# Performance work log

Hardware: AMD Instinct MI355X
Metric: run time of the kernel (lower is better)

The kernel has to match this reference:

```python
import jax, jax.numpy as jnp
import numpy as np

N, K, H, X_DIM, S_DIM = 50000, 8, 128, 32, 27
LSTM_IN = X_DIM + 3 * H  # 416


def setup_inputs() -> dict:
    key = jax.random.key(0)
    ks = jax.random.split(key, 16)

    def u(k, shape, fan_in):
        lim = 1.0 / np.sqrt(fan_in)
        return jax.random.uniform(k, shape, jnp.float32, -lim, lim)

    return {
        "x": jax.random.normal(ks[0], (N, X_DIM), jnp.float32),
        "h_self": jax.random.normal(ks[1], (N, H), jnp.float32),
        "c_self": jax.random.normal(ks[2], (N, H), jnp.float32),
        "h_inflows": jax.random.normal(ks[3], (N, K, H), jnp.float32),
        "inflow_valid": jax.random.randint(ks[4], (N, K), 0, 2) > 0,
        "static": jax.random.normal(ks[5], (N, S_DIM), jnp.float32),
        # Linear weights stored (out, in) as in eqx.nn.Linear
        "Wn": u(ks[6], (H, H), H),                     # W_neighbor, no bias
        "Wg": u(ks[7], (H, 2 * H), 2 * H),             # W_inflow_gate
        "bg": u(ks[8], (H,), 2 * H),
        "Ws": u(ks[9], (H, S_DIM), S_DIM),             # W_static
        "bs": u(ks[10], (H,), S_DIM),
        "Wl": u(ks[11], (4 * H, LSTM_IN), LSTM_IN),    # W_lstm
        "bl": u(ks[12], (4 * H,), LSTM_IN),
        "ln_w": jnp.ones((H,), jnp.float32),           # ln_h affine
        "ln_b": jnp.zeros((H,), jnp.float32),
    }


def reference(x, h_self, c_self, h_inflows, inflow_valid, static,
              Wn, Wg, bg, Ws, bs, Wl, bl, ln_w, ln_b):
    eps = 1e-5
    # per-neighbor message: [N,K,H]
    msgs = jnp.einsum('nkh,oh->nko', h_inflows, Wn)
    # inflow gate on concat(h_inflow, h_self): [N,K,H]
    h_tiled = jnp.broadcast_to(h_self[:, None, :], h_inflows.shape)
    gate_in = jnp.concatenate([h_inflows, h_tiled], axis=-1)  # [N,K,2H]
    gates = jax.nn.sigmoid(jnp.einsum('nkd,od->nko', gate_in, Wg) + bg)
    # masked sum over neighbors -> [N,H]
    mask = inflow_valid[..., None].astype(jnp.float32)
    neighbor_context = jnp.sum(gates * msgs * mask, axis=1)
    static_proj = static @ Ws.T + bs  # [N,H]
    combined = jnp.concatenate([x, h_self, neighbor_context, static_proj], axis=-1)
    z = combined @ Wl.T + bl  # [N,4H]
    i, f, o, g = jnp.split(z, 4, axis=-1)
    c_new = jax.nn.sigmoid(f) * c_self + jax.nn.sigmoid(i) * jnp.tanh(g)
    h_new = jax.nn.sigmoid(o) * jnp.tanh(c_new)
    # LayerNorm over hidden dim (eqx default eps=1e-5, affine)
    mu = jnp.mean(h_new, axis=-1, keepdims=True)
    var = jnp.mean(jnp.square(h_new - mu), axis=-1, keepdims=True)
    h_new = (h_new - mu) * jax.lax.rsqrt(var + eps) * ln_w + ln_b
    return (h_new, c_new)
```

## Files before the change

kernel.cpp:

```cpp
#include <hip/hip_runtime.h>
#include <hip/hip_bf16.h>

#define NN 50000
#define KI 8
#define H 128
#define XD 32
#define SD 27
#define CIN 416
#define CIN2 320
#define CPAD 328
#define ZOUT 512
#define NTILE_NB (NN / KI)
#define MB_LSTM 64

typedef __attribute__((ext_vector_type(8))) short bf16x8;
typedef __attribute__((ext_vector_type(4))) float f32x4;
typedef __attribute__((ext_vector_type(4))) unsigned short us4;

#define MFMA16(a, b, c) __builtin_amdgcn_mfma_f32_16x16x32_bf16((a), (b), (c), 0, 0, 0)

static __device__ __forceinline__ float sigmoidf_(float x) {
    return 1.0f / (1.0f + __expf(-x));
}
static __device__ __forceinline__ unsigned short f2b(float f) {
    union { float f; unsigned int u; } v; v.f = f;
    unsigned int r = v.u + 0x7FFF + ((v.u >> 16) & 1);
    return (unsigned short)(r >> 16);
}
static __device__ __forceinline__ float dot4_(float4 a, float4 b) {
    return a.x * b.x + a.y * b.y + a.z * b.z + a.w * b.w;
}

__global__ __launch_bounds__(256) void k_prep(
    const float* __restrict__ Wn, const float* __restrict__ Wg,
    const float* __restrict__ Wl, const float* __restrict__ bl,
    const float* __restrict__ Ws, const float* __restrict__ bs,
    unsigned short* __restrict__ WnB, unsigned short* __restrict__ WgB,
    unsigned short* __restrict__ WpB, float* __restrict__ bp)
{
    const int b = blockIdx.x, t = threadIdx.x;
    if (b < 512) {
        const float* wr = Wl + (size_t)b * CIN;
        unsigned short* out = WpB + (size_t)b * CIN2;
        for (int c = t; c < CIN2; c += 256) {
            float v;
            if (c < 288) v = wr[c];
            else if (c < 288 + SD) {
                int s = c - 288;
                float acc = 0.f;
                for (int j = 0; j < H; ++j) acc += wr[288 + j] * Ws[j * SD + s];
                v = acc;
            } else v = 0.f;
            out[c] = f2b(v);
        }
        if (t == 0) {
            float acc = bl[b];
            for (int j = 0; j < H; ++j) acc += wr[288 + j] * bs[j];
            bp[b] = acc;
        }
    } else {
        int idx = (b - 512) * 256 + t;
        for (int r = idx; r < 49152; r += 16384) {
            if (r < 16384) WnB[r] = f2b(Wn[r]);
            else WgB[r - 16384] = f2b(Wg[r - 16384]);
        }
    }
}

__global__ __launch_bounds__(256, 2) void k_nb_mfma(
    const float* __restrict__ hself_g, const float* __restrict__ hin_g,
    const unsigned char* __restrict__ valid_raw,
    const unsigned short* __restrict__ WnB, const unsigned short* __restrict__ WgB,
    const float* __restrict__ bg,
    unsigned short* __restrict__ ncb, int nc_stride)
{
    __shared__ unsigned short hin_s[64 * 128];
    __shared__ unsigned short hs_s[8 * 128];
    __shared__ float gh_s[8][128];
    __shared__ unsigned short ncs[8 * 128];
    __shared__ float valid_s[64];

    const int t = threadIdx.x;
    const int w = t >> 6, l = t & 63;
    const int ln = l & 15, lk = l >> 4;

    int det = 0;
    #pragma unroll
    for (int i = 0; i < 64; ++i) det |= valid_raw[4 * i + 1];
    const bool f8 = (det != 0);

    bf16x8 Bn[2][4], Ba[2][4], Bb[2][4];
    const int cbase = w * 32;
    #pragma unroll
    for (int c = 0; c < 2; ++c) {
        const int col = cbase + c * 16 + ln;
        #pragma unroll
        for (int kk = 0; kk < 4; ++kk) {
            const int k0 = kk * 32 + lk * 8;
            Bn[c][kk] = *(const bf16x8*)(WnB + col * H + k0);
            Ba[c][kk] = *(const bf16x8*)(WgB + col * 2 * H + k0);
            Bb[c][kk] = *(const bf16x8*)(WgB + col * 2 * H + H + k0);
        }
    }
    const float bg0 = bg[cbase + ln];
    const float bg1 = bg[cbase + 16 + ln];

    for (int tile = blockIdx.x; tile < NTILE_NB; tile += gridDim.x) {
        const int nb = tile * 8;

        if (t < 64) {
            bool v = f8 ? (valid_raw[(size_t)nb * KI + t] != 0)
                        : (((const unsigned int*)valid_raw)[(size_t)nb * KI + t] != 0u);
            valid_s[t] = v ? 1.f : 0.f;
        }
        {
            const float4* src = (const float4*)(hin_g + (size_t)nb * KI * H);
            float4 r0[8];
            #pragma unroll
            for (int i = 0; i < 8; ++i) r0[i] = src[t + i * 256];
            float4 hv = ((const float4*)(hself_g + (size_t)nb * H))[t];
            #pragma unroll
            for (int i = 0; i < 8; ++i) {
                int e = (t + i * 256) * 4, row = e >> 7, col = e & 127;
                unsigned byte = (unsigned)(row * 256 + col * 2) ^ (unsigned)((row & 7) << 4);
                us4 pk = { f2b(r0[i].x), f2b(r0[i].y), f2b(r0[i].z), f2b(r0[i].w) };
                *(us4*)((char*)hin_s + byte) = pk;
            }
            {
                int e = t * 4, row = e >> 7, col = e & 127;
                unsigned byte = (unsigned)(row * 256 + col * 2) ^ (unsigned)((row & 7) << 4);
                us4 pk = { f2b(hv.x), f2b(hv.y), f2b(hv.z), f2b(hv.w) };
                *(us4*)((char*)hs_s + byte) = pk;
            }
        }
        __syncthreads();

        f32x4 accM[4][2], accP[4][2], accG[2];
        #pragma unroll
        for (int m = 0; m < 4; ++m)
            #pragma unroll
            for (int c = 0; c < 2; ++c) { accM[m][c] = (f32x4)0.f; accP[m][c] = (f32x4)0.f; }
        accG[0] = (f32x4)0.f; accG[1] = (f32x4)0.f;

        #pragma unroll
        for (int kk = 0; kk < 4; ++kk) {
            const int k0 = kk * 32 + lk * 8;
            bf16x8 am[4];
            #pragma unroll
            for (int m = 0; m < 4; ++m) {
                int row = m * 16 + ln;
                unsigned byte = (unsigned)(row * 256 + k0 * 2) ^ (unsigned)((row & 7) << 4);
                am[m] = *(const bf16x8*)((const char*)hin_s + byte);
            }
            bf16x8 ah;
            {
                int row = ln & 7;
                unsigned byte = (unsigned)(row * 256 + k0 * 2) ^ (unsigned)((row & 7) << 4);
                ah = *(const bf16x8*)((const char*)hs_s + byte);
            }
            #pragma unroll
            for (int m = 0; m < 4; ++m)
                #pragma unroll
                for (int c = 0; c < 2; ++c) {
                    accM[m][c] = MFMA16(am[m], Bn[c][kk], accM[m][c]);
                    accP[m][c] = MFMA16(am[m], Ba[c][kk], accP[m][c]);
                }
            accG[0] = MFMA16(ah, Bb[0][kk], accG[0]);
            accG[1] = MFMA16(ah, Bb[1][kk], accG[1]);
        }

        #pragma unroll
        for (int c = 0; c < 2; ++c)
            #pragma unroll
            for (int r = 0; r < 4; ++r) {
                int row = lk * 4 + r;
                if (row < 8) gh_s[row][cbase + c * 16 + ln] = accG[c][r];
            }
        __syncthreads();

        #pragma unroll
        for (int m = 0; m < 4; ++m) {
            const int node = 2 * m + (lk >> 1);
            #pragma unroll
            for (int c = 0; c < 2; ++c) {
                const int col = cbase + c * 16 + ln;
                const float bgc = c ? bg1 : bg0;
                const float ghv = gh_s[node][col];
                float sum = 0.f;
                #pragma unroll
                for (int r = 0; r < 4; ++r) {
                    int row = m * 16 + lk * 4 + r;
                    float g = sigmoidf_(accP[m][c][r] + ghv + bgc);
                    sum += valid_s[row] * g * accM[m][c][r];
                }
                sum += __shfl_xor(sum, 16);
                if ((l & 16) == 0) ncs[(2 * m + (l >> 5)) * H + col] = f2b(sum);
            }
        }
        __syncthreads();

        {
            int e = t * 4, node = e >> 7, col = e & 127;
            us4 v = *(const us4*)(ncs + e);
            *(us4*)(ncb + (size_t)(nb + node) * nc_stride + col) = v;
        }
        __syncthreads();
    }
}

__global__ __launch_bounds__(256, 2) void k_lstm_mfma(
    const float* __restrict__ x_g, const float* __restrict__ hself_g,
    const float* __restrict__ cself_g, const float* __restrict__ stat_g,
    const unsigned short* __restrict__ ncb, int nc_stride,
    const unsigned short* __restrict__ WpB, const float* __restrict__ bp,
    const float* __restrict__ lnw, const float* __restrict__ lnb,
    float* __restrict__ h_out, float* __restrict__ c_out)
{
    __shared__ char smem[MB_LSTM * CPAD * 2];
    unsigned short* comb = (unsigned short*)smem;
    float (*hpre)[132] = (float(*)[132])smem;

    const int t = threadIdx.x;
    const int nb = blockIdx.x * MB_LSTM;
    const int w = t >> 6, l = t & 63, ln = l & 15, lk = l >> 4;

    #pragma unroll
    for (int i = 0; i < 2; ++i) {
        int p4 = t + i * 256;
        int e = p4 * 4, row = e >> 5, col = e & 31;
        us4 pk = { 0, 0, 0, 0 };
        if (nb + row < NN) {
            float4 v = ((const float4*)(x_g + (size_t)nb * XD))[p4];
            pk = us4{ f2b(v.x), f2b(v.y), f2b(v.z), f2b(v.w) };
        }
        *(us4*)(comb + row * CPAD + col) = pk;
    }
    #pragma unroll
    for (int i = 0; i < 8; ++i) {
        int p4 = t + i * 256;
        int e = p4 * 4, row = e >> 7, col = 32 + (e & 127);
        us4 pk = { 0, 0, 0, 0 };
        if (nb + row < NN) {
            float4 v = ((const float4*)(hself_g + (size_t)nb * H))[p4];
            pk = us4{ f2b(v.x), f2b(v.y), f2b(v.z), f2b(v.w) };
        }
        *(us4*)(comb + row * CPAD + col) = pk;
    }
    #pragma unroll
    for (int i = 0; i < 8; ++i) {
        int p4 = t + i * 256;
        int e = p4 * 4, row = e >> 7, col = e & 127;
        us4 v = { 0, 0, 0, 0 };
        if (nb + row < NN) v = *(const us4*)(ncb + (size_t)(nb + row) * nc_stride + col);
        *(us4*)(comb + row * CPAD + 160 + col) = v;
    }
    for (int i = t; i < MB_LSTM * SD; i += 256) {
        int row = i / SD, col = i - row * SD;
        unsigned short v = 0;
        if (nb + row < NN) v = f2b(stat_g[(size_t)(nb + row) * SD + col]);
        comb[row * CPAD + 288 + col] = v;
    }
    for (int i = t; i < MB_LSTM * (CPAD - 315); i += 256) {
        int nz = CPAD - 315;
        int row = i / nz, col = 315 + (i - row * nz);
        comb[row * CPAD + col] = 0;
    }
    __syncthreads();

    f32x4 acc[4][4][2];
    #pragma unroll
    for (int m = 0; m < 4; ++m)
        #pragma unroll
        for (int g = 0; g < 4; ++g) { acc[m][g][0] = (f32x4)0.f; acc[m][g][1] = (f32x4)0.f; }

    #pragma unroll
    for (int kk = 0; kk < 10; ++kk) {
        const int k0 = kk * 32 + lk * 8;
        bf16x8 a[4];
        #pragma unroll
        for (int m = 0; m < 4; ++m)
            a[m] = *(const bf16x8*)(comb + (m * 16 + ln) * CPAD + k0);
        #pragma unroll
        for (int g = 0; g < 4; ++g)
            #pragma unroll
            for (int p = 0; p < 2; ++p) {
                int zr = g * H + w * 32 + p * 16 + ln;
                bf16x8 b = *(const bf16x8*)(WpB + (size_t)zr * CIN2 + k0);
                #pragma unroll
                for (int m = 0; m < 4; ++m)
                    acc[m][g][p] = MFMA16(a[m], b, acc[m][g][p]);
            }
    }
    __syncthreads();

    #pragma unroll
    for (int p = 0; p < 2; ++p) {
        const int h = w * 32 + p * 16 + ln;
        const float bi = bp[h], bf = bp[H + h], bo = bp[2 * H + h], bgg = bp[3 * H + h];
        #pragma unroll
        for (int m = 0; m < 4; ++m)
            #pragma unroll
            for (int r = 0; r < 4; ++r) {
                int node = m * 16 + lk * 4 + r;
                size_t n = (size_t)(nb + node);
                if (n < NN) {
                    float zi = acc[m][0][p][r] + bi;
                    float zf = acc[m][1][p][r] + bf;
                    float zo = acc[m][2][p][r] + bo;
                    float zg = acc[m][3][p][r] + bgg;
                    float cn = sigmoidf_(zf) * cself_g[n * H + h] + sigmoidf_(zi) * tanhf(zg);
                    c_out[n * H + h] = cn;
                    hpre[node][h] = sigmoidf_(zo) * tanhf(cn);
                }
            }
    }
    __syncthreads();

    #pragma unroll
    for (int jj = 0; jj < 16; ++jj) {
        const int j = w * 16 + jj;
        const size_t n = (size_t)(nb + j);
        if (n < NN) {
            float a = hpre[j][l];
            float b = hpre[j][64 + l];
            float s = a + b, q = a * a + b * b;
            #pragma unroll
            for (int off = 1; off < 64; off <<= 1) {
                s += __shfl_xor(s, off);
                q += __shfl_xor(q, off);
            }
            float mu = s * (1.0f / 128.0f);
            float var = q * (1.0f / 128.0f) - mu * mu;
            float rstd = rsqrtf(var + 1e-5f);
            h_out[n * H + l]      = (a - mu) * rstd * lnw[l] + lnb[l];
            h_out[n * H + 64 + l] = (b - mu) * rstd * lnw[64 + l] + lnb[64 + l];
        }
    }
}

__global__ __launch_bounds__(256) void k_nb_f32(
    const float* __restrict__ hself_g, const float* __restrict__ hin_g,
    const unsigned char* __restrict__ valid_raw,
    const float* __restrict__ Wn, const float* __restrict__ Wg,
    const float* __restrict__ bg, float* __restrict__ nc)
{
    __shared__ float4 hin_s[8 * KI * (H / 4)];
    __shared__ float4 hs_s[8 * (H / 4)];
    __shared__ int flag8;
    const int t = threadIdx.x;
    const int nb = blockIdx.x * 8;
    {
        int loc = 0;
        if (t < 64) {
            #pragma unroll
            for (int i = 0; i < 16; ++i) loc |= valid_raw[4 * (t * 16 + i) + 1];
        }
        int any = __any(loc != 0);
        if (t == 0) flag8 = any;
    }
    const float4* src_hin = (const float4*)(hin_g + (size_t)nb * KI * H);
    #pragma unroll
    for (int i = 0; i < 8; ++i) hin_s[t + i * 256] = src_hin[t + i * 256];
    hs_s[t] = ((const float4*)(hself_g + (size_t)nb * H))[t];
    __syncthreads();
    const int o = t & 127, g = t >> 7;
    float msg[4][KI], gat[4][KI], gh[4];
    #pragma unroll
    for (int j = 0; j < 4; ++j) {
        gh[j] = 0.f;
        #pragma unroll
        for (int k = 0; k < KI; ++k) { msg[j][k] = 0.f; gat[j][k] = 0.f; }
    }
    const float4* Wn4 = (const float4*)(Wn + (size_t)o * H);
    const float4* Wg4a = (const float4*)(Wg + (size_t)o * 2 * H);
    const float4* Wg4b = (const float4*)(Wg + (size_t)o * 2 * H + H);
    for (int d4 = 0; d4 < H / 4; ++d4) {
        float4 wn = Wn4[d4], w0 = Wg4a[d4], w1 = Wg4b[d4];
        #pragma unroll
        for (int j = 0; j < 4; ++j) {
            const int node = g * 4 + j;
            gh[j] += dot4_(w1, hs_s[node * 32 + d4]);
            #pragma unroll
            for (int k = 0; k < KI; ++k) {
                float4 hv = hin_s[(node * KI + k) * 32 + d4];
                msg[j][k] += dot4_(wn, hv);
                gat[j][k] += dot4_(w0, hv);
            }
        }
    }
    const float bgo = bg[o];
    const unsigned int* valid32 = (const unsigned int*)valid_raw;
    const int f8 = flag8;
    #pragma unroll
    for (int j = 0; j < 4; ++j) {
        const int n = nb + g * 4 + j;
        float acc = 0.f;
        #pragma unroll
        for (int k = 0; k < KI; ++k) {
            bool v = f8 ? (valid_raw[n * KI + k] != 0) : (valid32[n * KI + k] != 0u);
            if (v) acc += sigmoidf_(gat[j][k] + gh[j] + bgo) * msg[j][k];
        }
        nc[(size_t)n * H + o] = acc;
    }
}

__global__ __launch_bounds__(256) void k_lstm_f32(
    const float* __restrict__ x_g, const float* __restrict__ hself_g,
    const float* __restrict__ cself_g, const float* __restrict__ stat_g,
    const float* __restrict__ nc,
    const float* __restrict__ Ws, const float* __restrict__ bs,
    const float* __restrict__ Wl, const float* __restrict__ bl,
    const float* __restrict__ lnw, const float* __restrict__ lnb,
    float* __restrict__ h_out, float* __restrict__ c_out)
{
    __shared__ float4 comb4[16 * (CIN / 4)];
    __shared__ float zsh[16 * ZOUT];
    __shared__ float stat_s[16 * SD];
    float* combf = (float*)comb4;
    const int t = threadIdx.x;
    const int nb = blockIdx.x * 16;
    #pragma unroll
    for (int i = 0; i < 2; ++i) {
        int idx = t + i * 256;
        combf[(idx >> 5) * CIN + (idx & 31)] = x_g[(size_t)nb * XD + idx];
    }
    #pragma unroll
    for (int i = 0; i < 8; ++i) {
        int idx = t + i * 256;
        combf[(idx >> 7) * CIN + 32 + (idx & 127)] = hself_g[(size_t)nb * H + idx];
    }
    #pragma unroll
    for (int i = 0; i < 8; ++i) {
        int idx = t + i * 256;
        combf[(idx >> 7) * CIN + 160 + (idx & 127)] = nc[(size_t)nb * H + idx];
    }
    stat_s[t] = stat_g[(size_t)nb * SD + t];
    if (t < 16 * SD - 256) stat_s[t + 256] = stat_g[(size_t)nb * SD + t + 256];
    __syncthreads();
    {
        const int o = t & 127, jg = t >> 7;
        #pragma unroll
        for (int jj = 0; jj < 8; ++jj) {
            const int j = jg * 8 + jj;
            float s = bs[o];
            #pragma unroll
            for (int c = 0; c < SD; ++c) s += Ws[o * SD + c] * stat_s[j * SD + c];
            combf[j * CIN + 288 + o] = s;
        }
    }
    __syncthreads();
    float acc0[16], acc1[16];
    #pragma unroll
    for (int j = 0; j < 16; ++j) { acc0[j] = 0.f; acc1[j] = 0.f; }
    const float4* W0 = (const float4*)(Wl + (size_t)t * CIN);
    const float4* W1 = (const float4*)(Wl + (size_t)(t + 256) * CIN);
    for (int d4 = 0; d4 < CIN / 4; ++d4) {
        float4 w0 = W0[d4], w1 = W1[d4];
        #pragma unroll
        for (int j = 0; j < 16; ++j) {
            float4 cv = comb4[j * (CIN / 4) + d4];
            acc0[j] += dot4_(w0, cv);
            acc1[j] += dot4_(w1, cv);
        }
    }
    const float bl0 = bl[t], bl1 = bl[t + 256];
    #pragma unroll
    for (int j = 0; j < 16; ++j) {
        zsh[j * ZOUT + t] = acc0[j] + bl0;
        zsh[j * ZOUT + 256 + t] = acc1[j] + bl1;
    }
    __syncthreads();
    {
        const int h = t & 127, jg = t >> 7;
        #pragma unroll
        for (int jj = 0; jj < 8; ++jj) {
            const int j = jg * 8 + jj;
            const size_t n = (size_t)(nb + j);
            float zi = zsh[j * ZOUT + h];
            float zf = zsh[j * ZOUT + 128 + h];
            float zo = zsh[j * ZOUT + 256 + h];
            float zg = zsh[j * ZOUT + 384 + h];
            float cn = sigmoidf_(zf) * cself_g[n * H + h] + sigmoidf_(zi) * tanhf(zg);
            c_out[n * H + h] = cn;
            zsh[j * ZOUT + h] = sigmoidf_(zo) * tanhf(cn);
        }
    }
    __syncthreads();
    {
        const int w = t >> 6, lane = t & 63;
        #pragma unroll
        for (int jj = 0; jj < 4; ++jj) {
            const int j = w * 4 + jj;
            const size_t n = (size_t)(nb + j);
            float a = zsh[j * ZOUT + lane];
            float b = zsh[j * ZOUT + 64 + lane];
            float s = a + b, q = a * a + b * b;
            #pragma unroll
            for (int off = 1; off < 64; off <<= 1) {
                s += __shfl_xor(s, off);
                q += __shfl_xor(q, off);
            }
            float mu = s * (1.0f / 128.0f);
            float var = q * (1.0f / 128.0f) - mu * mu;
            float rstd = rsqrtf(var + 1e-5f);
            h_out[n * H + lane] = (a - mu) * rstd * lnw[lane] + lnb[lane];
            h_out[n * H + 64 + lane] = (b - mu) * rstd * lnw[64 + lane] + lnb[64 + lane];
        }
    }
}

extern "C" void kernel_launch(void* const* d_in, const int* in_sizes, int n_in,
                              void* d_out, int out_size, void* d_ws, size_t ws_size,
                              hipStream_t stream) {
    const float* x      = (const float*)d_in[0];
    const float* h_self = (const float*)d_in[1];
    const float* c_self = (const float*)d_in[2];
    const float* h_inf  = (const float*)d_in[3];
    const unsigned char* valid = (const unsigned char*)d_in[4];
    const float* statp  = (const float*)d_in[5];
    const float* Wn     = (const float*)d_in[6];
    const float* Wg     = (const float*)d_in[7];
    const float* bg     = (const float*)d_in[8];
    const float* Ws     = (const float*)d_in[9];
    const float* bs     = (const float*)d_in[10];
    const float* Wl     = (const float*)d_in[11];
    const float* bl     = (const float*)d_in[12];
    const float* lnw    = (const float*)d_in[13];
    const float* lnb    = (const float*)d_in[14];

    float* h_out = (float*)d_out;
    float* c_out = h_out + (size_t)NN * H;

    const size_t W_BYTES = (size_t)512 * CIN2 * 2 + 16384 * 2 + 32768 * 2 + 512 * 4;
    const size_t NC_BYTES = (size_t)NN * H * 2;

    if (ws_size >= W_BYTES) {
        char* p = (char*)d_ws;
        unsigned short* WpB = (unsigned short*)p;           p += (size_t)512 * CIN2 * 2;
        unsigned short* WnB = (unsigned short*)p;           p += 16384 * 2;
        unsigned short* WgB = (unsigned short*)p;           p += 32768 * 2;
        float* bp = (float*)p;                              p += 512 * 4;

        unsigned short* ncb;
        int nc_stride;
        if (ws_size >= W_BYTES + NC_BYTES + 64) {
            ncb = (unsigned short*)p;
            nc_stride = H;
        } else {
            ncb = (unsigned short*)h_out;
            nc_stride = 256;
        }

        k_prep<<<576, 256, 0, stream>>>(Wn, Wg, Wl, bl, Ws, bs,
                                        WnB, WgB, WpB, bp);
        k_nb_mfma<<<512, 256, 0, stream>>>(h_self, h_inf, valid, WnB, WgB, bg,
                                           ncb, nc_stride);
        k_lstm_mfma<<<(NN + MB_LSTM - 1) / MB_LSTM, 256, 0, stream>>>(
            x, h_self, c_self, statp, ncb, nc_stride, WpB, bp,
            lnw, lnb, h_out, c_out);
    } else {
        float* nc_buf = (ws_size >= (size_t)NN * H * sizeof(float))
                            ? (float*)d_ws : h_out;
        k_nb_f32<<<NN / 8, 256, 0, stream>>>(h_self, h_inf, valid, Wn, Wg, bg, nc_buf);
        k_lstm_f32<<<NN / 16, 256, 0, stream>>>(x, h_self, c_self, statp, nc_buf,
                                                Ws, bs, Wl, bl, lnw, lnb, h_out, c_out);
    }
}
```

Before: 192.0 us.

## Shrink LSTM tile to 32 nodes with 512 threads and prefetch c_self

The LSTM MFMA kernel now processes 32 nodes per block using 8 waves of 512 threads, each wave owning 16 hidden columns, which cuts per-thread accumulator registers and raises the occupancy target. The c_self values are loaded into registers before the GEMM so their latency overlaps with it, and tanhf is replaced with an exp-based fast tanh. In exchange, each weight fragment is reused by only 2 M-tiles instead of 4, so weight traffic from L2 per node doubles.

Measured after the change: 180.8 us. 5.8% less time.

```diff
diff --git a/kernel.cpp b/kernel.cpp
--- a/kernel.cpp
+++ b/kernel.cpp
@@ -11,7 +11,7 @@
 #define CPAD 328
 #define ZOUT 512
 #define NTILE_NB (NN / KI)
-#define MB_LSTM 64
+#define MB_LSTM 32
 
 typedef __attribute__((ext_vector_type(8))) short bf16x8;
 typedef __attribute__((ext_vector_type(4))) float f32x4;
@@ -21,6 +21,9 @@
 
 static __device__ __forceinline__ float sigmoidf_(float x) {
     return 1.0f / (1.0f + __expf(-x));
+}
+static __device__ __forceinline__ float tanhf_(float x) {
+    return 1.0f - 2.0f / (__expf(2.0f * x) + 1.0f);
 }
 static __device__ __forceinline__ unsigned short f2b(float f) {
     union { float f; unsigned int u; } v; v.f = f;
@@ -208,7 +211,7 @@
     }
 }
 
-__global__ __launch_bounds__(256, 2) void k_lstm_mfma(
+__global__ __launch_bounds__(512, 4) void k_lstm_mfma(
     const float* __restrict__ x_g, const float* __restrict__ hself_g,
     const float* __restrict__ cself_g, const float* __restrict__ stat_g,
     const unsigned short* __restrict__ ncb, int nc_stride,
@@ -223,21 +226,20 @@
     const int t = threadIdx.x;
     const int nb = blockIdx.x * MB_LSTM;
     const int w = t >> 6, l = t & 63, ln = l & 15, lk = l >> 4;
-
-    #pragma unroll
-    for (int i = 0; i < 2; ++i) {
-        int p4 = t + i * 256;
-        int e = p4 * 4, row = e >> 5, col = e & 31;
+    const int hcol = w * 16 + ln;
+
+    if (t < 256) {
+        int e = t * 4, row = e >> 5, col = e & 31;
         us4 pk = { 0, 0, 0, 0 };
         if (nb + row < NN) {
-            float4 v = ((const float4*)(x_g + (size_t)nb * XD))[p4];
+            float4 v = ((const float4*)(x_g + (size_t)nb * XD))[t];
             pk = us4{ f2b(v.x), f2b(v.y), f2b(v.z), f2b(v.w) };
         }
         *(us4*)(comb + row * CPAD + col) = pk;
     }
     #pragma unroll
-    for (int i = 0; i < 8; ++i) {
-        int p4 = t + i * 256;
+    for (int i = 0; i < 2; ++i) {
+        int p4 = t + i * 512;
         int e = p4 * 4, row = e >> 7, col = 32 + (e & 127);
         us4 pk = { 0, 0, 0, 0 };
         if (nb + row < NN) {
@@ -247,78 +249,80 @@
         *(us4*)(comb + row * CPAD + col) = pk;
     }
     #pragma unroll
-    for (int i = 0; i < 8; ++i) {
-        int p4 = t + i * 256;
+    for (int i = 0; i < 2; ++i) {
+        int p4 = t + i * 512;
         int e = p4 * 4, row = e >> 7, col = e & 127;
         us4 v = { 0, 0, 0, 0 };
         if (nb + row < NN) v = *(const us4*)(ncb + (size_t)(nb + row) * nc_stride + col);
         *(us4*)(comb + row * CPAD + 160 + col) = v;
     }
-    for (int i = t; i < MB_LSTM * SD; i += 256) {
+    for (int i = t; i < MB_LSTM * SD; i += 512) {
         int row = i / SD, col = i - row * SD;
         unsigned short v = 0;
         if (nb + row < NN) v = f2b(stat_g[(size_t)(nb + row) * SD + col]);
         comb[row * CPAD + 288 + col] = v;
     }
-    for (int i = t; i < MB_LSTM * (CPAD - 315); i += 256) {
-        int nz = CPAD - 315;
-        int row = i / nz, col = 315 + (i - row * nz);
+    if (t < MB_LSTM * 5) {
+        int row = t / 5, col = 315 + t % 5;
         comb[row * CPAD + col] = 0;
     }
-    __syncthreads();
-
-    f32x4 acc[4][4][2];
-    #pragma unroll
-    for (int m = 0; m < 4; ++m)
-        #pragma unroll
-        for (int g = 0; g < 4; ++g) { acc[m][g][0] = (f32x4)0.f; acc[m][g][1] = (f32x4)0.f; }
+
+    float cpre[8];
+    #pragma unroll
+    for (int m = 0; m < 2; ++m)
+        #pragma unroll
+        for (int r = 0; r < 4; ++r) {
+            int node = m * 16 + lk * 4 + r;
+            size_t n = (size_t)(nb + node);
+            cpre[m * 4 + r] = (n < NN) ? cself_g[n * H + hcol] : 0.f;
+        }
+    __syncthreads();
+
+    f32x4 acc[2][4];
+    #pragma unroll
+    for (int m = 0; m < 2; ++m)
+        #pragma unroll
+        for (int g = 0; g < 4; ++g) acc[m][g] = (f32x4)0.f;
 
     #pragma unroll
     for (int kk = 0; kk < 10; ++kk) {
         const int k0 = kk * 32 + lk * 8;
-        bf16x8 a[4];
-        #pragma unroll
-        for (int m = 0; m < 4; ++m)
-            a[m] = *(const bf16x8*)(comb + (m * 16 + ln) * CPAD + k0);
-        #pragma unroll
-        for (int g = 0; g < 4; ++g)
-            #pragma unroll
-            for (int p = 0; p < 2; ++p) {
-                int zr = g * H + w * 32 + p * 16 + ln;
-                bf16x8 b = *(const bf16x8*)(WpB + (size_t)zr * CIN2 + k0);
-                #pragma unroll
-                for (int m = 0; m < 4; ++m)
-                    acc[m][g][p] = MFMA16(a[m], b, acc[m][g][p]);
-            }
-    }
-    __syncthreads();
-
-    #pragma unroll
-    for (int p = 0; p < 2; ++p) {
-        const int h = w * 32 + p * 16 + ln;
-        const float bi = bp[h], bf = bp[H + h], bo = bp[2 * H + h], bgg = bp[3 * H + h];
-        #pragma unroll
-        for (int m = 0; m < 4; ++m)
+        bf16x8 a0 = *(const bf16x8*)(comb + ln * CPAD + k0);
+        bf16x8 a1 = *(const bf16x8*)(comb + (16 + ln) * CPAD + k0);
+        #pragma unroll
+        for (int g = 0; g < 4; ++g) {
+            bf16x8 b = *(const bf16x8*)(WpB + (size_t)(g * H + hcol) * CIN2 + k0);
+            acc[0][g] = MFMA16(a0, b, acc[0][g]);
+            acc[1][g] = MFMA16(a1, b, acc[1][g]);
+        }
+    }
+    __syncthreads();
+
+    {
+        const float bi = bp[hcol], bf = bp[H + hcol];
+        const float bo = bp[2 * H + hcol], bgg = bp[3 * H + hcol];
+        #pragma unroll
+        for (int m = 0; m < 2; ++m)
             #pragma unroll
             for (int r = 0; r < 4; ++r) {
                 int node = m * 16 + lk * 4 + r;
                 size_t n = (size_t)(nb + node);
                 if (n < NN) {
-                    float zi = acc[m][0][p][r] + bi;
-                    float zf = acc[m][1][p][r] + bf;
-                    float zo = acc[m][2][p][r] + bo;
-                    float zg = acc[m][3][p][r] + bgg;
-                    float cn = sigmoidf_(zf) * cself_g[n * H + h] + sigmoidf_(zi) * tanhf(zg);
-                    c_out[n * H + h] = cn;
-                    hpre[node][h] = sigmoidf_(zo) * tanhf(cn);
+                    float zi = acc[m][0][r] + bi;
+                    float zf = acc[m][1][r] + bf;
+                    float zo = acc[m][2][r] + bo;
+                    float zg = acc[m][3][r] + bgg;
+                    float cn = sigmoidf_(zf) * cpre[m * 4 + r] + sigmoidf_(zi) * tanhf_(zg);
+                    c_out[n * H + hcol] = cn;
+                    hpre[node][hcol] = sigmoidf_(zo) * tanhf_(cn);
                 }
             }
     }
     __syncthreads();
 
     #pragma unroll
-    for (int jj = 0; jj < 16; ++jj) {
-        const int j = w * 16 + jj;
+    for (int jj = 0; jj < 4; ++jj) {
+        const int j = w * 4 + jj;
         const size_t n = (size_t)(nb + j);
         if (n < NN) {
             float a = hpre[j][l];
@@ -555,7 +559,7 @@
                                         WnB, WgB, WpB, bp);
         k_nb_mfma<<<512, 256, 0, stream>>>(h_self, h_inf, valid, WnB, WgB, bg,
                                            ncb, nc_stride);
-        k_lstm_mfma<<<(NN + MB_LSTM - 1) / MB_LSTM, 256, 0, stream>>>(
+        k_lstm_mfma<<<(NN + MB_LSTM - 1) / MB_LSTM, 512, 0, stream>>>(
             x, h_self, c_self, statp, ncb, nc_stride, WpB, bp,
             lnw, lnb, h_out, c_out);
     } else {
```
